# Optimization experiments

Hardware: AMD Instinct MI355X
Metric: run time of the kernel (lower is better)

## Reference

```python
import jax, jax.numpy as jnp
import numpy as np

B, SQ, SK, D, H = 4, 2048, 2048, 1024, 16
HD = D // H


def setup_inputs() -> dict:
    key = jax.random.key(0)
    ks = jax.random.split(key, 12)
    s = 1.0 / np.sqrt(D)
    return {
        "query": jax.random.normal(ks[0], (B, SQ, D), jnp.float32),
        "key": jax.random.normal(ks[1], (B, SK, D), jnp.float32),
        "value": jax.random.normal(ks[2], (B, SK, D), jnp.float32),
        "key_padding_mask": jax.random.randint(ks[3], (B, SK), 0, 2, jnp.int32),
        "Wq": jax.random.uniform(ks[4], (D, D), jnp.float32, -s, s),
        "bq": jnp.zeros((D,), jnp.float32),
        "Wk": jax.random.uniform(ks[5], (D, D), jnp.float32, -s, s),
        "bk": jnp.zeros((D,), jnp.float32),
        "Wv": jax.random.uniform(ks[6], (D, D), jnp.float32, -s, s),
        "bv": jnp.zeros((D,), jnp.float32),
        "Wo": jax.random.uniform(ks[7], (D, D), jnp.float32, -s, s),
        "bo": jnp.zeros((D,), jnp.float32),
    }


def reference(query, key, value, key_padding_mask, Wq, bq, Wk, bk, Wv, bv, Wo, bo):
    scale = HD ** -0.5
    # projections: torch Linear is x @ W.T + b
    q = (query @ Wq.T + bq).reshape(B, SQ, H, HD).transpose(0, 2, 1, 3)  # [B,H,SQ,HD]
    k = (key @ Wk.T + bk).reshape(B, SK, H, HD).transpose(0, 2, 1, 3)    # [B,H,SK,HD]
    v = (value @ Wv.T + bv).reshape(B, SK, H, HD).transpose(0, 2, 1, 3)  # [B,H,SK,HD]
    scores = jnp.einsum("bhqd,bhkd->bhqk", q, k) * scale                  # [B,H,SQ,SK]
    mask = key_padding_mask[:, None, None, :] != 0                        # True = keep
    scores = jnp.where(mask, scores, -jnp.inf)
    attn = jax.nn.softmax(scores, axis=-1)
    # dropout is identity at inference (eval mode)
    out = jnp.einsum("bhqk,bhkd->bhqd", attn, v)                          # [B,H,SQ,HD]
    out = out.transpose(0, 2, 1, 3).reshape(B, SQ, D)
    return out @ Wo.T + bo
```

## Files before the change

### kernel.cpp

```cpp
#include <hip/hip_runtime.h>


typedef __bf16 bf16_t;
typedef __attribute__((ext_vector_type(4))) __bf16 bf16x4;
typedef __attribute__((ext_vector_type(8))) __bf16 bf16x8;
typedef __attribute__((ext_vector_type(4))) float f32x4;

#define MFMA16(a, b, c) __builtin_amdgcn_mfma_f32_16x16x32_bf16(a, b, c, 0, 0, 0)

#define WAITV(N) asm volatile("s_waitcnt vmcnt(" #N ")" ::: "memory")

__device__ __forceinline__ void gl_lds16(const void* g, void* l) {
  __builtin_amdgcn_global_load_lds(
      (const __attribute__((address_space(1))) unsigned int*)g,
      (__attribute__((address_space(3))) unsigned int*)l, 16, 0, 0);
}

__device__ __forceinline__ void block_barrier() {
  asm volatile("" ::: "memory");
  __builtin_amdgcn_s_barrier();
  asm volatile("" ::: "memory");
}

__global__ void conv_kernel(const float* __restrict__ q, const float* __restrict__ k,
                            const float* __restrict__ v, const float* __restrict__ Wq,
                            const float* __restrict__ Wk, const float* __restrict__ Wv,
                            const float* __restrict__ Wo, bf16_t* __restrict__ q16,
                            bf16_t* __restrict__ k16, bf16_t* __restrict__ v16,
                            bf16_t* __restrict__ W16) {
  const int y = blockIdx.y;
  const float* src;
  bf16_t* dst;
  size_t idx;
  if (y < 3) {
    src = (y == 0) ? q : (y == 1) ? k : v;
    dst = (y == 0) ? q16 : (y == 1) ? k16 : v16;
    idx = ((size_t)blockIdx.x * 256 + threadIdx.x) * 4;
  } else {
    if (blockIdx.x >= 4096) return;
    const int m = blockIdx.x >> 10;
    src = (m == 0) ? Wq : (m == 1) ? Wk : (m == 2) ? Wv : Wo;
    dst = W16 + ((size_t)m << 20);
    idx = (((size_t)(blockIdx.x & 1023)) * 256 + threadIdx.x) * 4;
  }
  float4 w = *(const float4*)(src + idx);
  bf16x4 pk;
  pk[0] = (bf16_t)w.x; pk[1] = (bf16_t)w.y; pk[2] = (bf16_t)w.z; pk[3] = (bf16_t)w.w;
  *(bf16x4*)(dst + idx) = pk;
}

__global__ __launch_bounds__(256, 2) void gemm_kernel(
    const bf16_t* __restrict__ A0, const bf16_t* __restrict__ A1,
    const bf16_t* __restrict__ A2, const bf16_t* __restrict__ Wbase,
    const float* __restrict__ b0, const float* __restrict__ b1,
    const float* __restrict__ b2, void* __restrict__ o0, void* __restrict__ o1,
    void* __restrict__ o2, const int md0, const int md1, const int md2) {
  __shared__ __align__(16) bf16_t As[4][8 * 512];
  __shared__ __align__(16) bf16_t Bs[4][8 * 512];

  const int z = blockIdx.z;
  const bf16_t* A = (z == 0) ? A0 : (z == 1) ? A1 : A2;
  const bf16_t* Bw = Wbase + ((size_t)z << 20);
  const float* bias = (z == 0) ? b0 : (z == 1) ? b1 : b2;
  void* outp = (z == 0) ? o0 : (z == 1) ? o1 : o2;
  const int out_mode = (z == 0) ? md0 : (z == 1) ? md1 : md2;

  const int tid = threadIdx.x;
  const int lane = tid & 63, wave = tid >> 6;
  const int fm = lane & 15, quad = lane >> 4;
  const int wr = wave >> 1, wc = wave & 1;
  const int m0 = blockIdx.x * 128, n0 = blockIdx.y * 128;

  f32x4 acc[4][4];
#pragma unroll
  for (int i = 0; i < 4; ++i)
#pragma unroll
    for (int j = 0; j < 4; ++j) acc[i][j] = f32x4{0.f, 0.f, 0.f, 0.f};

  auto stage = [&](int ks, int buf) {
    const int k0 = ks * 32;
#pragma unroll
    for (int it = 0; it < 2; ++it) {
      const int fid = wave * 2 + it;
      gl_lds16(A + (size_t)(m0 + fid * 16 + fm) * 1024 + k0 + quad * 8,
               As[buf] + fid * 512);
    }
#pragma unroll
    for (int it = 0; it < 2; ++it) {
      const int fid = wave * 2 + it;
      gl_lds16(Bw + (size_t)(n0 + fid * 16 + fm) * 1024 + k0 + quad * 8,
               Bs[buf] + fid * 512);
    }
  };

  stage(0, 0);
  stage(1, 1);
  stage(2, 2);
  for (int ks = 0; ks < 32; ++ks) {
    if (ks <= 29) {
      WAITV(8);
    } else if (ks == 30) {
      WAITV(4);
    } else {
      WAITV(0);
    }
    block_barrier();
    if (ks + 3 < 32) stage(ks + 3, (ks + 3) & 3);
    const bf16_t* Ab = As[ks & 3];
    const bf16_t* Bb = Bs[ks & 3];
    bf16x8 af[4], bfr[4];
#pragma unroll
    for (int i = 0; i < 4; ++i)
      af[i] = *(const bf16x8*)(Ab + (4 * wr + i) * 512 + lane * 8);
#pragma unroll
    for (int j = 0; j < 4; ++j)
      bfr[j] = *(const bf16x8*)(Bb + (4 * wc + j) * 512 + lane * 8);
#pragma unroll
    for (int i = 0; i < 4; ++i)
#pragma unroll
      for (int j = 0; j < 4; ++j) acc[i][j] = MFMA16(af[i], bfr[j], acc[i][j]);
  }

  float bval[4];
#pragma unroll
  for (int j = 0; j < 4; ++j) bval[j] = bias[n0 + wc * 64 + j * 16 + fm];

#pragma unroll
  for (int i = 0; i < 4; ++i) {
#pragma unroll
    for (int j = 0; j < 4; ++j) {
      const int col = n0 + wc * 64 + j * 16 + fm;
#pragma unroll
      for (int r = 0; r < 4; ++r) {
        const int row = m0 + wr * 64 + i * 16 + quad * 4 + r;
        const float v = acc[i][j][r] + bval[j];
        if (out_mode == 2) {
          ((float*)outp)[(size_t)row * 1024 + col] = v;
        } else if (out_mode == 0) {
          ((bf16_t*)outp)[(size_t)row * 1024 + col] = (bf16_t)v;
        } else {
          const int bb = row >> 11, sk = row & 2047;
          const int tt = sk >> 7, L128 = sk & 127;
          const int c = L128 >> 5, hf = (L128 >> 4) & 1;
          const int qd = (L128 >> 2) & 3, rr = L128 & 3;
          const int hh = col >> 6, hd = col & 63;
          const int nt = hd >> 4, fv = hd & 15;
          const size_t idx = (((size_t)(bb * 16 + hh)) << 17) + tt * 8192 +
                             (nt * 4 + c) * 512 + (qd * 16 + fv) * 8 + hf * 4 + rr;
          ((bf16_t*)outp)[idx] = (bf16_t)v;
        }
      }
    }
  }
}

__global__ __launch_bounds__(256, 2) void attn_kernel(
    const bf16_t* __restrict__ q16, const bf16_t* __restrict__ k16,
    const bf16_t* __restrict__ vt16, const int* __restrict__ mask,
    bf16_t* __restrict__ o16) {
  __shared__ __align__(16) bf16_t Kb[2][8192];
  __shared__ __align__(16) bf16_t Vb[2][8192];
  __shared__ float mbuf[2][128];
  __shared__ float lbuf[128];

  const int tid = threadIdx.x;
  const int lane = tid & 63, wave = tid >> 6;
  const int fm = lane & 15, quad = lane >> 4;
  const int lin = blockIdx.y * 16 + blockIdx.x;
  const int xcd = lin & 7, slot = lin >> 3;
  const int qt = slot & 15;
  const int bh = ((slot >> 4) << 3) + xcd;
  const int b = bh >> 4, h = bh & 15;
  const float SC = 0.125f * 1.44269504f;

  bf16x8 aq[2][2];
#pragma unroll
  for (int i = 0; i < 2; ++i)
#pragma unroll
    for (int dc = 0; dc < 2; ++dc) {
      const int row = qt * 128 + (2 * wave + i) * 16 + fm;
      aq[i][dc] = *(const bf16x8*)(q16 + ((size_t)(b * 2048 + row)) * 1024 + h * 64 +
                                   dc * 32 + quad * 8);
    }

  auto stageKV = [&](int t, int buf) {
    const bf16_t* kb = k16 + ((size_t)(b * 2048 + t * 128)) * 1024 + h * 64;
#pragma unroll
    for (int s = 0; s < 4; ++s) {
      const int fid = wave * 4 + s;
      const int row = (fid >> 1) * 16 + fm;
      const int col = (fid & 1) * 32 + quad * 8;
      gl_lds16(kb + (size_t)row * 1024 + col, Kb[buf] + fid * 512);
    }
    const bf16_t* vbase = vt16 + ((size_t)bh << 17) + t * 8192;
#pragma unroll
    for (int s = 0; s < 4; ++s) {
      const int fid = wave * 4 + s;
      gl_lds16(vbase + fid * 512 + lane * 8, Vb[buf] + fid * 512);
    }
    if (tid < 128) mbuf[buf][tid] = mask[b * 2048 + t * 128 + tid] ? 0.0f : -1e30f;
  };

  f32x4 oacc[2][4];
#pragma unroll
  for (int i = 0; i < 2; ++i)
#pragma unroll
    for (int n = 0; n < 4; ++n) oacc[i][n] = f32x4{0.f, 0.f, 0.f, 0.f};
  float lrow[2] = {0.f, 0.f};

  stageKV(0, 0);
  for (int t = 0; t < 16; ++t) {
    __syncthreads();
    if (t + 1 < 16) stageKV(t + 1, (t + 1) & 1);
    const bf16_t* K = Kb[t & 1];
    const bf16_t* V = Vb[t & 1];
    const float* mb = mbuf[t & 1];

    f32x4 sacc[2][8];
#pragma unroll
    for (int i = 0; i < 2; ++i)
#pragma unroll
      for (int j = 0; j < 8; ++j) sacc[i][j] = f32x4{0.f, 0.f, 0.f, 0.f};
#pragma unroll
    for (int j = 0; j < 8; ++j) {
#pragma unroll
      for (int dc = 0; dc < 2; ++dc) {
        bf16x8 kf = *(const bf16x8*)(K + (j * 2 + dc) * 512 + lane * 8);
        sacc[0][j] = MFMA16(kf, aq[0][dc], sacc[0][j]);
        sacc[1][j] = MFMA16(kf, aq[1][dc], sacc[1][j]);
      }
    }

#pragma unroll
    for (int j = 0; j < 8; ++j) {
      f32x4 md = *(const f32x4*)&mb[j * 16 + quad * 4];
#pragma unroll
      for (int i = 0; i < 2; ++i) {
#pragma unroll
        for (int r = 0; r < 4; ++r) {
          const float p = __builtin_amdgcn_exp2f(fmaf(sacc[i][j][r], SC, md[r]));
          sacc[i][j][r] = p;
          lrow[i] += p;
        }
      }
    }

#pragma unroll
    for (int c = 0; c < 4; ++c) {
      bf16x8 pf[2];
#pragma unroll
      for (int i = 0; i < 2; ++i) {
#pragma unroll
        for (int r = 0; r < 4; ++r) {
          pf[i][r] = (bf16_t)sacc[i][2 * c][r];
          pf[i][4 + r] = (bf16_t)sacc[i][2 * c + 1][r];
        }
      }
#pragma unroll
      for (int n = 0; n < 4; ++n) {
        bf16x8 vv = *(const bf16x8*)(V + (n * 4 + c) * 512 + lane * 8);
        oacc[0][n] = MFMA16(pf[0], vv, oacc[0][n]);
        oacc[1][n] = MFMA16(pf[1], vv, oacc[1][n]);
      }
    }
  }

#pragma unroll
  for (int i = 0; i < 2; ++i) {
    float l = lrow[i];
    l += __shfl_xor(l, 16);
    l += __shfl_xor(l, 32);
    if (quad == 0) lbuf[wave * 32 + i * 16 + fm] = l;
  }
  __syncthreads();
#pragma unroll
  for (int i = 0; i < 2; ++i) {
    f32x4 lv = *(const f32x4*)&lbuf[wave * 32 + i * 16 + quad * 4];
#pragma unroll
    for (int r = 0; r < 4; ++r) {
      const float inv = 1.0f / lv[r];
      const int row = qt * 128 + wave * 32 + i * 16 + quad * 4 + r;
#pragma unroll
      for (int n = 0; n < 4; ++n) {
        o16[((size_t)(b * 2048 + row)) * 1024 + h * 64 + n * 16 + fm] =
            (bf16_t)(oacc[i][n][r] * inv);
      }
    }
  }
}

extern "C" void kernel_launch(void* const* d_in, const int* in_sizes, int n_in,
                              void* d_out, int out_size, void* d_ws, size_t ws_size,
                              hipStream_t stream) {
  const float* query = (const float*)d_in[0];
  const float* key   = (const float*)d_in[1];
  const float* value = (const float*)d_in[2];
  const int* mask    = (const int*)d_in[3];
  const float* Wq = (const float*)d_in[4];
  const float* bq = (const float*)d_in[5];
  const float* Wk = (const float*)d_in[6];
  const float* bk = (const float*)d_in[7];
  const float* Wv = (const float*)d_in[8];
  const float* bv = (const float*)d_in[9];
  const float* Wo = (const float*)d_in[10];
  const float* bo = (const float*)d_in[11];

  const size_t MB = 1024 * 1024;
  char* ws = (char*)d_ws;
  bf16_t* W16 = (bf16_t*)ws;
  bf16_t* qin = (bf16_t*)(ws + 8 * MB);
  bf16_t* kin = (bf16_t*)(ws + 24 * MB);
  bf16_t* vin = (bf16_t*)(ws + 40 * MB);
  bf16_t* q16 = (bf16_t*)(ws + 56 * MB);

  bf16_t* k16  = (bf16_t*)d_out;
  bf16_t* vt16 = (bf16_t*)((char*)d_out + 16 * MB);
  bf16_t* o16  = qin;

  conv_kernel<<<dim3(8192, 4), 256, 0, stream>>>(query, key, value, Wq, Wk, Wv, Wo,
                                                 qin, kin, vin, W16);

  gemm_kernel<<<dim3(64, 8, 3), 256, 0, stream>>>(
      qin, kin, vin, W16, bq, bk, bv, q16, k16, vt16, 0, 0, 1);

  attn_kernel<<<dim3(16, 64), 256, 0, stream>>>(q16, k16, vt16, mask, o16);

  gemm_kernel<<<dim3(64, 8, 1), 256, 0, stream>>>(
      o16, nullptr, nullptr, W16 + 3145728, bo, nullptr, nullptr, d_out, nullptr,
      nullptr, 2, 0, 0);
}
```

Before: 394.8 us.

## Split-K the output projection GEMM and cut pipeline depth for occupancy

The output projection GEMM is split along K into two halves run as separate z-slices, each writing fp32 partials, then a new elementwise kernel adds the partial buffer into the output. The GEMM pipeline drops from 4 LDS buffers to 3 with launch bounds raised to 3 blocks per SM, which increases occupancy but shortens prefetch depth. The split doubles block count for the 512-block output GEMM to fill more CUs, at the cost of an extra 16MB fp32 write/read and an additional kernel launch.

Result: slower. 408.3 us (+3.4%).

```diff
diff --git a/kernel.cpp b/kernel.cpp
--- a/kernel.cpp
+++ b/kernel.cpp
@@ -49,21 +49,33 @@
   *(bf16x4*)(dst + idx) = pk;
 }
 
-__global__ __launch_bounds__(256, 2) void gemm_kernel(
+__global__ void addp_kernel(float* __restrict__ dst, const float* __restrict__ src) {
+  const size_t idx = ((size_t)blockIdx.x * 256 + threadIdx.x) * 4;
+  float4 a = *(const float4*)(dst + idx);
+  float4 b = *(const float4*)(src + idx);
+  a.x += b.x; a.y += b.y; a.z += b.z; a.w += b.w;
+  *(float4*)(dst + idx) = a;
+}
+
+template <int NSTEP>
+__global__ __launch_bounds__(256, 3) void gemm_kernel(
     const bf16_t* __restrict__ A0, const bf16_t* __restrict__ A1,
-    const bf16_t* __restrict__ A2, const bf16_t* __restrict__ Wbase,
+    const bf16_t* __restrict__ A2, const bf16_t* __restrict__ W0,
+    const bf16_t* __restrict__ W1, const bf16_t* __restrict__ W2,
     const float* __restrict__ b0, const float* __restrict__ b1,
     const float* __restrict__ b2, void* __restrict__ o0, void* __restrict__ o1,
-    void* __restrict__ o2, const int md0, const int md1, const int md2) {
-  __shared__ __align__(16) bf16_t As[4][8 * 512];
-  __shared__ __align__(16) bf16_t Bs[4][8 * 512];
+    void* __restrict__ o2, const int md0, const int md1, const int md2,
+    const int kb0, const int kb1, const int kb2) {
+  __shared__ __align__(16) bf16_t As[3][8 * 512];
+  __shared__ __align__(16) bf16_t Bs[3][8 * 512];
 
   const int z = blockIdx.z;
   const bf16_t* A = (z == 0) ? A0 : (z == 1) ? A1 : A2;
-  const bf16_t* Bw = Wbase + ((size_t)z << 20);
+  const bf16_t* Bw = (z == 0) ? W0 : (z == 1) ? W1 : W2;
   const float* bias = (z == 0) ? b0 : (z == 1) ? b1 : b2;
   void* outp = (z == 0) ? o0 : (z == 1) ? o1 : o2;
   const int out_mode = (z == 0) ? md0 : (z == 1) ? md1 : md2;
+  const int kbase = (z == 0) ? kb0 : (z == 1) ? kb1 : kb2;
 
   const int tid = threadIdx.x;
   const int lane = tid & 63, wave = tid >> 6;
@@ -78,7 +90,7 @@
     for (int j = 0; j < 4; ++j) acc[i][j] = f32x4{0.f, 0.f, 0.f, 0.f};
 
   auto stage = [&](int ks, int buf) {
-    const int k0 = ks * 32;
+    const int k0 = kbase + ks * 32;
 #pragma unroll
     for (int it = 0; it < 2; ++it) {
       const int fid = wave * 2 + it;
@@ -95,19 +107,17 @@
 
   stage(0, 0);
   stage(1, 1);
-  stage(2, 2);
-  for (int ks = 0; ks < 32; ++ks) {
-    if (ks <= 29) {
-      WAITV(8);
-    } else if (ks == 30) {
+  int cur = 0, stg = 2;
+  for (int ks = 0; ks < NSTEP; ++ks) {
+    if (ks < NSTEP - 1) {
       WAITV(4);
     } else {
       WAITV(0);
     }
     block_barrier();
-    if (ks + 3 < 32) stage(ks + 3, (ks + 3) & 3);
-    const bf16_t* Ab = As[ks & 3];
-    const bf16_t* Bb = Bs[ks & 3];
+    if (ks + 2 < NSTEP) stage(ks + 2, stg);
+    const bf16_t* Ab = As[cur];
+    const bf16_t* Bb = Bs[cur];
     bf16x8 af[4], bfr[4];
 #pragma unroll
     for (int i = 0; i < 4; ++i)
@@ -119,11 +129,14 @@
     for (int i = 0; i < 4; ++i)
 #pragma unroll
       for (int j = 0; j < 4; ++j) acc[i][j] = MFMA16(af[i], bfr[j], acc[i][j]);
+    cur = (cur == 2) ? 0 : cur + 1;
+    stg = (stg == 2) ? 0 : stg + 1;
   }
 
   float bval[4];
 #pragma unroll
-  for (int j = 0; j < 4; ++j) bval[j] = bias[n0 + wc * 64 + j * 16 + fm];
+  for (int j = 0; j < 4; ++j)
+    bval[j] = bias ? bias[n0 + wc * 64 + j * 16 + fm] : 0.0f;
 
 #pragma unroll
   for (int i = 0; i < 4; ++i) {
@@ -316,16 +329,20 @@
   bf16_t* k16  = (bf16_t*)d_out;
   bf16_t* vt16 = (bf16_t*)((char*)d_out + 16 * MB);
   bf16_t* o16  = qin;
+  float*  pw   = (float*)(ws + 24 * MB);
 
   conv_kernel<<<dim3(8192, 4), 256, 0, stream>>>(query, key, value, Wq, Wk, Wv, Wo,
                                                  qin, kin, vin, W16);
 
-  gemm_kernel<<<dim3(64, 8, 3), 256, 0, stream>>>(
-      qin, kin, vin, W16, bq, bk, bv, q16, k16, vt16, 0, 0, 1);
+  gemm_kernel<32><<<dim3(64, 8, 3), 256, 0, stream>>>(
+      qin, kin, vin, W16, W16 + 1048576, W16 + 2097152, bq, bk, bv,
+      q16, k16, vt16, 0, 0, 1, 0, 0, 0);
 
   attn_kernel<<<dim3(16, 64), 256, 0, stream>>>(q16, k16, vt16, mask, o16);
 
-  gemm_kernel<<<dim3(64, 8, 1), 256, 0, stream>>>(
-      o16, nullptr, nullptr, W16 + 3145728, bo, nullptr, nullptr, d_out, nullptr,
-      nullptr, 2, 0, 0);
-}
+  gemm_kernel<16><<<dim3(64, 8, 2), 256, 0, stream>>>(
+      o16, o16, nullptr, W16 + 3145728, W16 + 3145728, nullptr, bo, nullptr,
+      nullptr, d_out, pw, nullptr, 2, 2, 0, 0, 512, 0);
+
+  addp_kernel<<<8192, 256, 0, stream>>>((float*)d_out, pw);
+}
```
